# Performance work log

Hardware: AMD Instinct MI355X
Metric: run time of the kernel (lower is better)

Reference implementation:

```python
import jax, jax.numpy as jnp
import numpy as np

NUM_HEADS = 16
KEY_DIM = 128
VALUE_DIM = 128
HIDDEN = 2048


def setup_inputs() -> dict:
    key = jax.random.key(0)
    k1, k2, k3 = jax.random.split(key, 3)
    B, T = 4, 2048
    hidden_states = jax.random.normal(k1, (B, T, HIDDEN), dtype=jnp.float32)
    # qkv_proj: Linear(hidden, H*(2*key_dim+value_dim)) no bias -> weight (out, in)
    qkv_out = NUM_HEADS * (2 * KEY_DIM + VALUE_DIM)
    w_qkv = jax.random.normal(k2, (qkv_out, HIDDEN), dtype=jnp.float32) * (1.0 / np.sqrt(HIDDEN))
    w_out = jax.random.normal(k3, (HIDDEN, NUM_HEADS * VALUE_DIM), dtype=jnp.float32) * (1.0 / np.sqrt(NUM_HEADS * VALUE_DIM))
    b_out = jnp.zeros((HIDDEN,), dtype=jnp.float32)
    return {"hidden_states": hidden_states, "w_qkv": w_qkv, "w_out": w_out, "b_out": b_out}


def reference(hidden_states, w_qkv, w_out, b_out):
    B, T, _ = hidden_states.shape
    H, Dk, Dv = NUM_HEADS, KEY_DIM, VALUE_DIM
    scale = 1.0 / np.sqrt(Dk).astype(np.float32)
    qkv = hidden_states @ w_qkv.T  # (B,T,H*(2Dk+Dv))
    q, k, v = jnp.split(qkv, [H * Dk, 2 * H * Dk], axis=-1)
    q = q.reshape(B, T, H, Dk).transpose(0, 2, 1, 3)  # (B,H,T,Dk)
    k = k.reshape(B, T, H, Dk).transpose(0, 2, 1, 3)
    v = v.reshape(B, T, H, Dv).transpose(0, 2, 1, 3)
    scores = jnp.einsum('bhtd,bhsd->bhts', q, k) * scale  # (B,H,T,S)
    causal = jnp.tril(jnp.ones((T, T), dtype=bool))
    scores = jnp.where(causal[None, None], scores, jnp.float32(-jnp.inf))
    attn = jax.nn.softmax(scores, axis=-1)
    out = jnp.einsum('bhts,bhsd->bhtd', attn, v)  # (B,H,T,Dv)
    out = out.transpose(0, 2, 1, 3).reshape(B, T, H * Dv)
    return out @ w_out.T + b_out
```

## Files before the change

### kernel.cpp

```cpp
#include <hip/hip_runtime.h>
#include <hip/hip_bf16.h>
#include <stdint.h>

#define HID   2048
#define NH    16
#define QKV_N 6144
#define QKP   4096
#define BT    8192
#define TT    2048

typedef short bf16x8  __attribute__((ext_vector_type(8)));
typedef float f32x4   __attribute__((ext_vector_type(4)));
typedef float f32x16  __attribute__((ext_vector_type(16)));
typedef unsigned short u16;

__device__ __forceinline__ u16 f2bf(float f){
  union { float f; unsigned u; } v; v.f = f;
  unsigned r = 0x7fffu + ((v.u >> 16) & 1u);
  return (u16)((v.u + r) >> 16);
}
__device__ __forceinline__ float bf2f(u16 x){
  union { unsigned u; float f; } v; v.u = ((unsigned)x) << 16;
  return v.f;
}
__device__ __forceinline__ unsigned cvt_pk_bf16(float lo, float hi){
  unsigned r;
  asm("v_cvt_pk_bf16_f32 %0, %1, %2" : "=v"(r) : "v"(lo), "v"(hi));
  return r;
}

typedef __attribute__((address_space(3))) void lds_vt;
typedef const __attribute__((address_space(1))) void gbl_vt;

__device__ __forceinline__ void gload16(const void* g, void* l){
  __builtin_amdgcn_global_load_lds((gbl_vt*)g, (lds_vt*)l, 16, 0, 0);
}

#define FENCE() asm volatile("" ::: "memory")
#define SYNC()  { FENCE(); __builtin_amdgcn_s_barrier(); FENCE(); }

__global__ __launch_bounds__(256) void cvt_all(const float* __restrict__ in1, u16* __restrict__ o1, int n1,
                                               const float* __restrict__ in2, u16* __restrict__ o2, int n2,
                                               const float* __restrict__ in3, u16* __restrict__ o3, int n3){
  int i = blockIdx.x * blockDim.x + threadIdx.x;
  const int stride = gridDim.x * blockDim.x;
  const int ntot = n1 + n2 + n3;
  for (; i < ntot; i += stride){
    const float* ip; u16* op; int k;
    if (i < n1)            { ip = in1; op = o1; k = i; }
    else if (i < n1 + n2)  { ip = in2; op = o2; k = i - n1; }
    else                   { ip = in3; op = o3; k = i - n1 - n2; }
    float4 v = ((const float4*)ip)[k];
    ushort4 o;
    o.x = f2bf(v.x); o.y = f2bf(v.y); o.z = f2bf(v.z); o.w = f2bf(v.w);
    ((ushort4*)op)[k] = o;
  }
}

template<int MODE>
__global__ __launch_bounds__(512, 2) void gemm256(const u16* __restrict__ A,
                                                  const u16* __restrict__ Bm,
                                                  u16* __restrict__ Cb,
                                                  float* __restrict__ Cf,
                                                  const float* __restrict__ bias,
                                                  u16* __restrict__ vt2,
                                                  int M, int N, int K)
{
  __shared__ u16 lds[4 * 256 * 64];
  u16* const Abuf[2] = { lds,          lds + 16384 };
  u16* const Bbuf[2] = { lds + 32768,  lds + 49152 };

  const int tid  = threadIdx.x;
  const int w    = tid >> 6;
  const int lane = tid & 63;
  const int wm   = w >> 2;
  const int wn   = w & 3;
  const int lr   = lane & 15;
  const int lg   = lane >> 4;

  int bid = blockIdx.x;
  { int qq = gridDim.x >> 3; bid = (bid & 7) * qq + (bid >> 3); }
  const int ntile = N >> 8;
  const int m0 = (bid / ntile) << 8;
  const int n0 = (bid % ntile) << 8;

  const int rS = tid >> 3;
  const int cS = ((tid & 7) ^ (rS & 7)) * 8;
  const u16* gA = A  + (size_t)(m0 + rS) * K + cS;
  const u16* gB = Bm + (size_t)(n0 + rS) * K + cS;
  const int wds = w * 512;

  f32x4 acc[8][4] = {};
  bf16x8 aq[2][2], bq[4][2];

  auto stgA = [&](int buf, int half, int kt){
    const u16* s = gA + (size_t)(half * 128) * K + (size_t)kt * 64;
    gload16(s,                  Abuf[buf] + half * 8192 + wds);
    gload16(s + (size_t)64 * K, Abuf[buf] + half * 8192 + 4096 + wds);
  };
  auto stgB = [&](int buf, int half, int kt){
    const u16* s = gB + (size_t)(half * 128) * K + (size_t)kt * 64;
    gload16(s,                  Bbuf[buf] + half * 8192 + wds);
    gload16(s + (size_t)64 * K, Bbuf[buf] + half * 8192 + 4096 + wds);
  };
  auto loadA = [&](const u16* ab, int q){
    #pragma unroll
    for (int kk = 0; kk < 2; ++kk){
      #pragma unroll
      for (int mf2 = 0; mf2 < 2; ++mf2){
        int row = wm * 128 + (q * 2 + mf2) * 16 + lr;
        int blk = (kk * 4 + lg) ^ (lr & 7);
        aq[mf2][kk] = *(const bf16x8*)(ab + row * 64 + blk * 8);
      }
    }
  };
  auto loadB = [&](const u16* bb){
    #pragma unroll
    for (int nf = 0; nf < 4; ++nf){
      #pragma unroll
      for (int kk = 0; kk < 2; ++kk){
        int row = wn * 64 + nf * 16 + lr;
        int blk = (kk * 4 + lg) ^ (lr & 7);
        bq[nf][kk] = *(const bf16x8*)(bb + row * 64 + blk * 8);
      }
    }
  };

#define MFMAQ(Q) do {                                                         \
    __builtin_amdgcn_s_setprio(1);                                            \
    _Pragma("unroll")                                                         \
    for (int kk = 0; kk < 2; ++kk){                                           \
      _Pragma("unroll")                                                       \
      for (int mf2 = 0; mf2 < 2; ++mf2){                                      \
        _Pragma("unroll")                                                     \
        for (int nf = 0; nf < 4; ++nf)                                        \
          acc[(Q)*2+mf2][nf] = __builtin_amdgcn_mfma_f32_16x16x32_bf16(       \
              aq[mf2][kk], bq[nf][kk], acc[(Q)*2+mf2][nf], 0, 0, 0);          \
      }                                                                       \
    }                                                                         \
    __builtin_amdgcn_s_setprio(0);                                            \
  } while (0)

  stgA(0, 0, 0); stgA(0, 1, 0);
  stgB(0, 0, 0); stgB(0, 1, 0);
  stgB(1, 0, 1); stgB(1, 1, 1);
  asm volatile("s_waitcnt vmcnt(4)" ::: "memory");
  SYNC();

  const int NI = K >> 7;
  for (int it = 0; it < NI; ++it){
    const int t = it * 2;
    const bool lastI = (it == NI - 1);

    loadB(Bbuf[0]);
    loadA(Abuf[0], 0);
    stgA(1, 0, t + 1);
    SYNC(); MFMAQ(0); SYNC();

    loadA(Abuf[0], 1);
    stgA(1, 1, t + 1);
    SYNC(); MFMAQ(1); SYNC();

    loadA(Abuf[0], 2);
    if (!lastI) stgB(0, 0, t + 2);
    SYNC(); MFMAQ(2); SYNC();

    loadA(Abuf[0], 3);
    if (!lastI) stgB(0, 1, t + 2);
    SYNC(); MFMAQ(3);
    if (lastI) asm volatile("s_waitcnt vmcnt(0)" ::: "memory");
    else       asm volatile("s_waitcnt vmcnt(4)" ::: "memory");
    SYNC();

    loadB(Bbuf[1]);
    loadA(Abuf[1], 0);
    if (!lastI) stgA(0, 0, t + 2);
    SYNC(); MFMAQ(0); SYNC();

    loadA(Abuf[1], 1);
    if (!lastI) stgA(0, 1, t + 2);
    SYNC(); MFMAQ(1); SYNC();

    loadA(Abuf[1], 2);
    if (!lastI) stgB(1, 0, t + 3);
    SYNC(); MFMAQ(2); SYNC();

    loadA(Abuf[1], 3);
    if (!lastI) stgB(1, 1, t + 3);
    SYNC(); MFMAQ(3);
    if (!lastI) asm volatile("s_waitcnt vmcnt(4)" ::: "memory");
    SYNC();
  }
#undef MFMAQ

  const int orow = m0 + wm * 128 + lg * 4;
  const int ocol = n0 + wn * 64 + lr;

  if (MODE == 1 && n0 >= 4096){
    #pragma unroll
    for (int nf = 0; nf < 4; ++nf){
      const int c   = ocol + nf * 16 - 4096;
      const int h2  = c >> 7;
      const int d   = c & 127;
      const int r64 = d & 63;
      const int hd  = d >> 6;
      #pragma unroll
      for (int mf = 0; mf < 8; ++mf)
        #pragma unroll
        for (int r = 0; r < 4; ++r){
          const int row = orow + mf * 16 + r;
          const int bb  = row >> 11;
          const int t   = row & 2047;
          const int t5  = t >> 5;
          const int kv  = t & 31;
          const int sl  = hd * 4 + (kv >> 3);
          const int sp  = sl ^ (r64 & 7);
          vt2[(size_t)((bb * 16 + h2) * 64 + t5) * 4096 + r64 * 64 + sp * 8 + (kv & 7)]
              = f2bf(acc[mf][nf][r]);
        }
    }
  } else {
    #pragma unroll
    for (int mf = 0; mf < 8; ++mf)
      #pragma unroll
      for (int nf = 0; nf < 4; ++nf)
        #pragma unroll
        for (int r = 0; r < 4; ++r){
          int row = orow + mf * 16 + r;
          int col = ocol + nf * 16;
          float v = acc[mf][nf][r];
          if (MODE == 1)
            Cb[(size_t)row * QKP + col] = f2bf(v);
          else
            Cf[(size_t)row * N + col] = v + bias[col];
        }
  }
}

__global__ __launch_bounds__(256, 3) void attn(const u16* __restrict__ qk,
                                               const u16* __restrict__ vt2,
                                               u16* __restrict__ aout)
{
  __shared__ u16 Kl[3][32 * 128];
  __shared__ u16 Vl[3][64 * 64];

  const int qt = 15 - (int)blockIdx.y;
  const int bh = blockIdx.x;
  const int b = bh >> 4, h = bh & 15;
  const int tid  = threadIdx.x;
  const int w    = tid >> 6;
  const int lane = tid & 63;
  const int l31  = lane & 31;
  const int hi   = lane >> 5;
  const int sw7  = l31 & 7;

  const int qg = qt * 128 + w * 32 + l31;
  const float sc2 = 0.08838834764831845f * 1.4426950408889634f;

  bf16x8 qf[8];
  {
    const u16* qp = qk + (size_t)(b * TT + qg) * QKP + h * 128 + hi * 8;
    #pragma unroll
    for (int s = 0; s < 8; ++s){
      bf16x8 raw = *(const bf16x8*)(qp + s * 16);
      unsigned pk[4];
      #pragma unroll
      for (int p2 = 0; p2 < 4; ++p2)
        pk[p2] = cvt_pk_bf16(bf2f((u16)raw[2 * p2]) * sc2,
                             bf2f((u16)raw[2 * p2 + 1]) * sc2);
      int4 u = { (int)pk[0], (int)pk[1], (int)pk[2], (int)pk[3] };
      qf[s] = *(bf16x8*)&u;
    }
  }

  f32x16 o[4] = {};
  float lsum = 0.f;

  const u16* ksrc = qk + (size_t)(b * TT + (tid >> 4)) * QKP + 2048 + h * 128
                    + (((tid & 15) ^ ((tid >> 4) & 7)) * 8);
  const u16* vsrc = vt2 + (size_t)bh * (64 * 4096) + tid * 8;

  auto stage = [&](int buf, int j){
    const u16* ks = ksrc + (size_t)(j * 32) * QKP;
    gload16(ks,                    &Kl[buf][tid * 8]);
    gload16(ks + (size_t)16 * QKP, &Kl[buf][2048 + tid * 8]);
    const u16* vs = vsrc + (size_t)j * 4096;
    gload16(vs,        &Vl[buf][tid * 8]);
    gload16(vs + 2048, &Vl[buf][2048 + tid * 8]);
  };

  const int NT  = 4 * qt + 4;
  const int jme = qt * 4 + w;
  stage(0, 0);
  stage(1, 1);

  int cur = 0;
  for (int j = 0; j < NT; ++j){
    SYNC();
    if (j + 2 < NT){
      int nb = cur + 2; if (nb >= 3) nb -= 3;
      stage(nb, j + 2);
      asm volatile("s_waitcnt vmcnt(8)" ::: "memory");
    } else if (j + 1 < NT){
      asm volatile("s_waitcnt vmcnt(4)" ::: "memory");
    } else {
      asm volatile("s_waitcnt vmcnt(0)" ::: "memory");
    }
    SYNC();

    if (j <= jme){
      f32x16 sa = {}, sb = {};
      const u16* KB = Kl[cur];
      __builtin_amdgcn_s_setprio(1);
      #pragma unroll
      for (int sl = 0; sl < 4; ++sl){
        const int spa = ((sl * 2 + hi) ^ sw7) * 8;
        const int spb = (((sl + 4) * 2 + hi) ^ sw7) * 8;
        bf16x8 ka = *(const bf16x8*)(KB + l31 * 128 + spa);
        bf16x8 kb2 = *(const bf16x8*)(KB + l31 * 128 + spb);
        sa = __builtin_amdgcn_mfma_f32_32x32x16_bf16(ka,  qf[sl],     sa, 0, 0, 0);
        sb = __builtin_amdgcn_mfma_f32_32x32x16_bf16(kb2, qf[sl + 4], sb, 0, 0, 0);
      }
      __builtin_amdgcn_s_setprio(0);

      f32x16 s;
      #pragma unroll
      for (int r = 0; r < 16; ++r) s[r] = sa[r] + sb[r];

      if (j == jme){
        #pragma unroll
        for (int r = 0; r < 16; ++r){
          const int krow = (r & 3) + 8 * (r >> 2) + 4 * hi;
          if (krow > l31) s[r] = -3.0e38f;
        }
      }

      #pragma unroll
      for (int r = 0; r < 16; ++r) s[r] = exp2f(s[r]);
      {
        float t0 = (s[0] + s[1]) + (s[2] + s[3]);
        float t1 = (s[4] + s[5]) + (s[6] + s[7]);
        float t2 = (s[8] + s[9]) + (s[10] + s[11]);
        float t3 = (s[12] + s[13]) + (s[14] + s[15]);
        lsum += (t0 + t1) + (t2 + t3);
      }

      bf16x8 pf[2];
      #pragma unroll
      for (int kb = 0; kb < 2; ++kb){
        const int R0 = kb * 8;
        const unsigned wa0 = cvt_pk_bf16(s[R0],     s[R0 + 1]);
        const unsigned wa1 = cvt_pk_bf16(s[R0 + 2], s[R0 + 3]);
        const unsigned wb0 = cvt_pk_bf16(s[R0 + 4], s[R0 + 5]);
        const unsigned wb1 = cvt_pk_bf16(s[R0 + 6], s[R0 + 7]);
        const int s0 = hi ? (int)wa0 : (int)wb0;
        const int s1 = hi ? (int)wa1 : (int)wb1;
        const int r0 = __shfl_xor(s0, 32, 64);
        const int r1 = __shfl_xor(s1, 32, 64);
        int4 u;
        u.x = hi ? r0 : (int)wa0;
        u.y = hi ? r1 : (int)wa1;
        u.z = hi ? (int)wb0 : r0;
        u.w = hi ? (int)wb1 : r1;
        pf[kb] = *(bf16x8*)&u;
      }

      const u16* VB = Vl[cur];
      __builtin_amdgcn_s_setprio(1);
      #pragma unroll
      for (int db = 0; db < 4; ++db){
        const int r6 = (db & 1) * 32 + l31;
        const int hd = db >> 1;
        #pragma unroll
        for (int kb = 0; kb < 2; ++kb){
          const int sp = ((hd * 4 + kb * 2 + hi) ^ sw7) * 8;
          bf16x8 vf = *(const bf16x8*)(VB + r6 * 64 + sp);
          o[db] = __builtin_amdgcn_mfma_f32_32x32x16_bf16(vf, pf[kb], o[db], 0, 0, 0);
        }
      }
      __builtin_amdgcn_s_setprio(0);
    }

    ++cur; if (cur == 3) cur = 0;
  }

  const float lt = lsum + __shfl_xor(lsum, 32, 64);
  const float inv = 1.0f / lt;
  u16* op = aout + (size_t)(b * TT + qg) * HID + h * 128;
  #pragma unroll
  for (int db = 0; db < 4; ++db)
    #pragma unroll
    for (int rq = 0; rq < 4; ++rq){
      ushort4 pk;
      pk.x = f2bf(o[db][rq * 4 + 0] * inv);
      pk.y = f2bf(o[db][rq * 4 + 1] * inv);
      pk.z = f2bf(o[db][rq * 4 + 2] * inv);
      pk.w = f2bf(o[db][rq * 4 + 3] * inv);
      *(ushort4*)(op + db * 32 + rq * 8 + hi * 4) = pk;
    }
}

extern "C" void kernel_launch(void* const* d_in, const int* in_sizes, int n_in,
                              void* d_out, int out_size, void* d_ws, size_t ws_size,
                              hipStream_t stream)
{
  (void)in_sizes; (void)n_in; (void)out_size; (void)ws_size;
  const float* hs    = (const float*)d_in[0];
  const float* w_qkv = (const float*)d_in[1];
  const float* w_out = (const float*)d_in[2];
  const float* b_out = (const float*)d_in[3];
  float* out = (float*)d_out;

  char* ws = (char*)d_ws;
  u16* qk_bf   = (u16*)(ws);
  u16* vt2_bf  = (u16*)(ws + 67108864);
  u16* wout_bf = (u16*)(ws + 100663296);
  u16* hs_bf   = (u16*)(ws + 109051904);
  u16* attn_bf = hs_bf;
  u16* wqkv_bf = (u16*)(ws + 142606336);

  cvt_all<<<4096, 256, 0, stream>>>(hs,    hs_bf,   (BT * HID) / 4,
                                    w_qkv, wqkv_bf, (QKV_N * HID) / 4,
                                    w_out, wout_bf, (HID * 2048) / 4);

  gemm256<1><<<(BT / 256) * (QKV_N / 256), 512, 0, stream>>>(
      hs_bf, wqkv_bf, qk_bf, nullptr, nullptr, vt2_bf, BT, QKV_N, HID);

  attn<<<dim3(64, 16), 256, 0, stream>>>(qk_bf, vt2_bf, attn_bf);

  gemm256<0><<<(BT / 256) * (HID / 256), 512, 0, stream>>>(
      attn_bf, wout_bf, nullptr, out, b_out, nullptr, BT, HID, HID);
}
```

Before: 362.6 us.

## Switch attention K/V staging to double-buffered 64-key tiles

```diff
diff --git a/kernel.cpp b/kernel.cpp
--- a/kernel.cpp
+++ b/kernel.cpp
@@ -237,12 +237,12 @@
   }
 }
 
-__global__ __launch_bounds__(256, 3) void attn(const u16* __restrict__ qk,
+__global__ __launch_bounds__(256, 2) void attn(const u16* __restrict__ qk,
                                                const u16* __restrict__ vt2,
                                                u16* __restrict__ aout)
 {
-  __shared__ u16 Kl[3][32 * 128];
-  __shared__ u16 Vl[3][64 * 64];
+  __shared__ u16 Kl[2][64 * 128];
+  __shared__ u16 Vl[2][2][4096];
 
   const int qt = 15 - (int)blockIdx.y;
   const int bh = blockIdx.x;
@@ -281,107 +281,109 @@
   const u16* vsrc = vt2 + (size_t)bh * (64 * 4096) + tid * 8;
 
   auto stage = [&](int buf, int j){
-    const u16* ks = ksrc + (size_t)(j * 32) * QKP;
-    gload16(ks,                    &Kl[buf][tid * 8]);
-    gload16(ks + (size_t)16 * QKP, &Kl[buf][2048 + tid * 8]);
-    const u16* vs = vsrc + (size_t)j * 4096;
-    gload16(vs,        &Vl[buf][tid * 8]);
-    gload16(vs + 2048, &Vl[buf][2048 + tid * 8]);
+    const u16* ks = ksrc + (size_t)(j * 64) * QKP;
+    #pragma unroll
+    for (int i = 0; i < 4; ++i)
+      gload16(ks + (size_t)(i * 16) * QKP, &Kl[buf][i * 2048 + tid * 8]);
+    const u16* vs = vsrc + (size_t)(2 * j) * 4096;
+    #pragma unroll
+    for (int s = 0; s < 2; ++s){
+      gload16(vs + s * 4096,        &Vl[buf][s][tid * 8]);
+      gload16(vs + s * 4096 + 2048, &Vl[buf][s][2048 + tid * 8]);
+    }
   };
 
-  const int NT  = 4 * qt + 4;
-  const int jme = qt * 4 + w;
+  const int NT    = 2 * qt + 2;
+  const int jme32 = qt * 4 + w;
   stage(0, 0);
-  stage(1, 1);
-
-  int cur = 0;
+
   for (int j = 0; j < NT; ++j){
+    const int cur = j & 1;
     SYNC();
-    if (j + 2 < NT){
-      int nb = cur + 2; if (nb >= 3) nb -= 3;
-      stage(nb, j + 2);
+    if (j + 1 < NT){
+      stage(cur ^ 1, j + 1);
       asm volatile("s_waitcnt vmcnt(8)" ::: "memory");
-    } else if (j + 1 < NT){
-      asm volatile("s_waitcnt vmcnt(4)" ::: "memory");
     } else {
       asm volatile("s_waitcnt vmcnt(0)" ::: "memory");
     }
     SYNC();
 
-    if (j <= jme){
-      f32x16 sa = {}, sb = {};
-      const u16* KB = Kl[cur];
-      __builtin_amdgcn_s_setprio(1);
-      #pragma unroll
-      for (int sl = 0; sl < 4; ++sl){
-        const int spa = ((sl * 2 + hi) ^ sw7) * 8;
-        const int spb = (((sl + 4) * 2 + hi) ^ sw7) * 8;
-        bf16x8 ka = *(const bf16x8*)(KB + l31 * 128 + spa);
-        bf16x8 kb2 = *(const bf16x8*)(KB + l31 * 128 + spb);
-        sa = __builtin_amdgcn_mfma_f32_32x32x16_bf16(ka,  qf[sl],     sa, 0, 0, 0);
-        sb = __builtin_amdgcn_mfma_f32_32x32x16_bf16(kb2, qf[sl + 4], sb, 0, 0, 0);
+    #pragma unroll
+    for (int sb = 0; sb < 2; ++sb){
+      const int jj = 2 * j + sb;
+      if (jj <= jme32){
+        f32x16 sa = {}, sbv = {};
+        const u16* KB = &Kl[cur][sb * 4096];
+        __builtin_amdgcn_s_setprio(1);
+        #pragma unroll
+        for (int sl = 0; sl < 4; ++sl){
+          const int spa = ((sl * 2 + hi) ^ sw7) * 8;
+          const int spb = (((sl + 4) * 2 + hi) ^ sw7) * 8;
+          bf16x8 ka  = *(const bf16x8*)(KB + l31 * 128 + spa);
+          bf16x8 kb2 = *(const bf16x8*)(KB + l31 * 128 + spb);
+          sa  = __builtin_amdgcn_mfma_f32_32x32x16_bf16(ka,  qf[sl],     sa,  0, 0, 0);
+          sbv = __builtin_amdgcn_mfma_f32_32x32x16_bf16(kb2, qf[sl + 4], sbv, 0, 0, 0);
+        }
+        __builtin_amdgcn_s_setprio(0);
+
+        f32x16 s;
+        #pragma unroll
+        for (int r = 0; r < 16; ++r) s[r] = sa[r] + sbv[r];
+
+        if (jj == jme32){
+          #pragma unroll
+          for (int r = 0; r < 16; ++r){
+            const int krow = (r & 3) + 8 * (r >> 2) + 4 * hi;
+            if (krow > l31) s[r] = -3.0e38f;
+          }
+        }
+
+        #pragma unroll
+        for (int r = 0; r < 16; ++r) s[r] = exp2f(s[r]);
+        {
+          float t0 = (s[0] + s[1]) + (s[2] + s[3]);
+          float t1 = (s[4] + s[5]) + (s[6] + s[7]);
+          float t2 = (s[8] + s[9]) + (s[10] + s[11]);
+          float t3 = (s[12] + s[13]) + (s[14] + s[15]);
+          lsum += (t0 + t1) + (t2 + t3);
+        }
+
+        bf16x8 pf[2];
+        #pragma unroll
+        for (int kb = 0; kb < 2; ++kb){
+          const int R0 = kb * 8;
+          const unsigned wa0 = cvt_pk_bf16(s[R0],     s[R0 + 1]);
+          const unsigned wa1 = cvt_pk_bf16(s[R0 + 2], s[R0 + 3]);
+          const unsigned wb0 = cvt_pk_bf16(s[R0 + 4], s[R0 + 5]);
+          const unsigned wb1 = cvt_pk_bf16(s[R0 + 6], s[R0 + 7]);
+          const int s0 = hi ? (int)wa0 : (int)wb0;
+          const int s1 = hi ? (int)wa1 : (int)wb1;
+          const int r0 = __shfl_xor(s0, 32, 64);
+          const int r1 = __shfl_xor(s1, 32, 64);
+          int4 u;
+          u.x = hi ? r0 : (int)wa0;
+          u.y = hi ? r1 : (int)wa1;
+          u.z = hi ? (int)wb0 : r0;
+          u.w = hi ? (int)wb1 : r1;
+          pf[kb] = *(bf16x8*)&u;
+        }
+
+        const u16* VB = Vl[cur][sb];
+        __builtin_amdgcn_s_setprio(1);
+        #pragma unroll
+        for (int db = 0; db < 4; ++db){
+          const int r6 = (db & 1) * 32 + l31;
+          const int hd = db >> 1;
+          #pragma unroll
+          for (int kb = 0; kb < 2; ++kb){
+            const int sp = ((hd * 4 + kb * 2 + hi) ^ sw7) * 8;
+            bf16x8 vf = *(const bf16x8*)(VB + r6 * 64 + sp);
+            o[db] = __builtin_amdgcn_mfma_f32_32x32x16_bf16(vf, pf[kb], o[db], 0, 0, 0);
+          }
+        }
+        __builtin_amdgcn_s_setprio(0);
       }
-      __builtin_amdgcn_s_setprio(0);
-
-      f32x16 s;
-      #pragma unroll
-      for (int r = 0; r < 16; ++r) s[r] = sa[r] + sb[r];
-
-      if (j == jme){
-        #pragma unroll
-        for (int r = 0; r < 16; ++r){
-          const int krow = (r & 3) + 8 * (r >> 2) + 4 * hi;
-          if (krow > l31) s[r] = -3.0e38f;
-        }
-      }
-
-      #pragma unroll
-      for (int r = 0; r < 16; ++r) s[r] = exp2f(s[r]);
-      {
-        float t0 = (s[0] + s[1]) + (s[2] + s[3]);
-        float t1 = (s[4] + s[5]) + (s[6] + s[7]);
-        float t2 = (s[8] + s[9]) + (s[10] + s[11]);
-        float t3 = (s[12] + s[13]) + (s[14] + s[15]);
-        lsum += (t0 + t1) + (t2 + t3);
-      }
-
-      bf16x8 pf[2];
-      #pragma unroll
-      for (int kb = 0; kb < 2; ++kb){
-        const int R0 = kb * 8;
-        const unsigned wa0 = cvt_pk_bf16(s[R0],     s[R0 + 1]);
-        const unsigned wa1 = cvt_pk_bf16(s[R0 + 2], s[R0 + 3]);
-        const unsigned wb0 = cvt_pk_bf16(s[R0 + 4], s[R0 + 5]);
-        const unsigned wb1 = cvt_pk_bf16(s[R0 + 6], s[R0 + 7]);
-        const int s0 = hi ? (int)wa0 : (int)wb0;
-        const int s1 = hi ? (int)wa1 : (int)wb1;
-        const int r0 = __shfl_xor(s0, 32, 64);
-        const int r1 = __shfl_xor(s1, 32, 64);
-        int4 u;
-        u.x = hi ? r0 : (int)wa0;
-        u.y = hi ? r1 : (int)wa1;
-        u.z = hi ? (int)wb0 : r0;
-        u.w = hi ? (int)wb1 : r1;
-        pf[kb] = *(bf16x8*)&u;
-      }
-
-      const u16* VB = Vl[cur];
-      __builtin_amdgcn_s_setprio(1);
-      #pragma unroll
-      for (int db = 0; db < 4; ++db){
-        const int r6 = (db & 1) * 32 + l31;
-        const int hd = db >> 1;
-        #pragma unroll
-        for (int kb = 0; kb < 2; ++kb){
-          const int sp = ((hd * 4 + kb * 2 + hi) ^ sw7) * 8;
-          bf16x8 vf = *(const bf16x8*)(VB + r6 * 64 + sp);
-          o[db] = __builtin_amdgcn_mfma_f32_32x32x16_bf16(vf, pf[kb], o[db], 0, 0, 0);
-        }
-      }
-      __builtin_amdgcn_s_setprio(0);
-    }
-
-    ++cur; if (cur == 3) cur = 0;
+    }
   }
 
   const float lt = lsum + __shfl_xor(lsum, 32, 64);
```

Measured after the change: 367.5 us. About the same (+1.4%).
